# Performance work log

Hardware: AMD Instinct MI355X
Metric: run time of the kernel (lower is better)

## Reference

```python
import jax, jax.numpy as jnp
import numpy as np

HIDDEN = 1024
EMB = HIDDEN // 2          # embedding_dim = hidden_dim // 2
NUM_OPS = 8
BATCH = 16384


def setup_inputs() -> dict:
    key = jax.random.key(0)
    ks = jax.random.split(key, 8)
    x = jax.random.normal(ks[0], (BATCH, HIDDEN), dtype=jnp.float32)
    sampled_ops = jax.random.randint(ks[1], (BATCH,), 0, NUM_OPS, dtype=jnp.int32)
    op_emb = jax.random.normal(ks[2], (NUM_OPS, EMB), dtype=jnp.float32) * 0.02
    # per-expert 2-layer MLP params (Linear stored as [in, out] for x @ W)
    s1 = 1.0 / np.sqrt(HIDDEN + EMB)
    s2 = 1.0 / np.sqrt(HIDDEN)
    W1 = jax.random.uniform(ks[3], (NUM_OPS, HIDDEN + EMB, HIDDEN), jnp.float32, -s1, s1)
    b1 = jax.random.uniform(ks[4], (NUM_OPS, HIDDEN), jnp.float32, -s1, s1)
    W2 = jax.random.uniform(ks[5], (NUM_OPS, HIDDEN, HIDDEN), jnp.float32, -s2, s2)
    b2 = jax.random.uniform(ks[6], (NUM_OPS, HIDDEN), jnp.float32, -s2, s2)
    return {"x": x, "sampled_ops": sampled_ops, "op_emb": op_emb,
            "W1": W1, "b1": b1, "W2": W2, "b2": b2}


def reference(x, sampled_ops, op_emb, W1, b1, W2, b2):
    # gather per-token operator embedding and augment input
    emb = jnp.take(op_emb, sampled_ops, axis=0)            # [B, EMB]
    x_aug = jnp.concatenate([x, emb], axis=-1)             # [B, H+EMB]
    num_ops = W1.shape[0]
    out = jnp.zeros_like(x)
    # loop over the small fixed expert set; mask-combine per token
    for o in range(num_ops):
        h = jax.nn.relu(x_aug @ W1[o] + b1[o])             # [B, H]
        y = jax.nn.relu(h @ W2[o] + b2[o])                 # [B, H]
        mask = (sampled_ops == o)[:, None]
        out = out + jnp.where(mask, y, 0.0)
    return out
```

## Files before the change

### kernel.cpp

```cpp
#include <hip/hip_runtime.h>
#include <hip/hip_bf16.h>

#define BATCH 16384
#define HID   1024
#define EMBD  512
#define NOPS  8
#define MAXT  136
#define CNTS  16

typedef __attribute__((ext_vector_type(8))) short bf16x8;
typedef __attribute__((ext_vector_type(4))) float f32x4;

__device__ __forceinline__ unsigned short f2bf(float f) {
  unsigned int u = __float_as_uint(f);
  u += 0x7FFF + ((u >> 16) & 1);
  return (unsigned short)(u >> 16);
}

__device__ __forceinline__ unsigned int pk2(float a, float b) {
  __hip_bfloat162 t = __float22bfloat162_rn(make_float2(a, b));
  return *(unsigned int*)(&t);
}

__device__ __forceinline__ void lds_load16(void* lds, const void* g) {
  __builtin_amdgcn_global_load_lds(
      (const __attribute__((address_space(1))) unsigned int*)g,
      (__attribute__((address_space(3))) unsigned int*)lds, 16, 0, 0);
}

__device__ __forceinline__ void decode_bid(int bid, int& g, int& nx) {
  g = 17 * (bid & 7) + (bid >> 6);
  nx = (bid >> 3) & 7;
}

__device__ __forceinline__ void w_prep_tile(const float* __restrict__ W,
                                            short* __restrict__ Wp,
                                            int ks, int nx, int tid) {
  int n = tid & 127, kh = tid >> 7;
  const float* src = W + (size_t)(ks * 32 + kh * 16) * 1024 + nx * 128 + n;
  float v[16];
#pragma unroll
  for (int kk = 0; kk < 16; ++kk) v[kk] = src[(size_t)kk * 1024];
  uint4 a, b;
  a.x = pk2(v[0], v[1]);  a.y = pk2(v[2], v[3]);
  a.z = pk2(v[4], v[5]);  a.w = pk2(v[6], v[7]);
  b.x = pk2(v[8], v[9]);  b.y = pk2(v[10], v[11]);
  b.z = pk2(v[12], v[13]); b.w = pk2(v[14], v[15]);
  uint4* dst = (uint4*)Wp;
  dst[(2 * kh) * 128 + n]     = a;
  dst[(2 * kh + 1) * 128 + n] = b;
}

__global__ void bucket_ce_k(const int* __restrict__ ops, int* __restrict__ cnt,
                            int* __restrict__ idx, const float* __restrict__ W1,
                            const float* __restrict__ emb,
                            const float* __restrict__ b1, float* __restrict__ ce,
                            short* __restrict__ W1p, const float* __restrict__ x,
                            unsigned int* __restrict__ xb) {
  int bid = blockIdx.x;
  int tid = threadIdx.x;
  if (bid >= 2240) {
    size_t i = ((size_t)(bid - 2240) * 256 + tid) * 16;
    const float4* src = (const float4*)(x + i);
    float4 f0 = src[0], f1 = src[1], f2v = src[2], f3 = src[3];
    uint4 p0 = make_uint4(pk2(f0.x, f0.y), pk2(f0.z, f0.w),
                          pk2(f1.x, f1.y), pk2(f1.z, f1.w));
    uint4 p1 = make_uint4(pk2(f2v.x, f2v.y), pk2(f2v.z, f2v.w),
                          pk2(f3.x, f3.y), pk2(f3.z, f3.w));
    uint4* dst = (uint4*)(xb + i / 2);
    dst[0] = p0;
    dst[1] = p1;
    return;
  }
  if (bid >= 192) {
    int b = bid - 192;
    int e = b / 256; int rr = b % 256; int nx = rr / 32, ks = rr % 32;
    w_prep_tile(W1 + (size_t)e * 1536 * 1024,
                W1p + ((size_t)(e * 8 + nx) * 32 + ks) * 4096, ks, nx, tid);
    return;
  }
  if (bid >= 64) {
    int cb = bid - 64;
    int e = cb >> 4, kp = cb & 15;
    int n = tid * 4;
    const float* Wc = W1 + (size_t)e * 1536 * 1024 + (size_t)(1024 + kp * 32) * 1024 + n;
    const float* ee = emb + e * EMBD + kp * 32;
    float4 a = make_float4(0.f, 0.f, 0.f, 0.f);
#pragma unroll
    for (int kk = 0; kk < 32; ++kk) {
      float s = ee[kk];
      float4 r = *(const float4*)(Wc + (size_t)kk * 1024);
      a.x += s * r.x; a.y += s * r.y; a.z += s * r.z; a.w += s * r.w;
    }
    if (kp == 0) {
      float4 b = *(const float4*)(b1 + e * HID + n);
      a.x += b.x; a.y += b.y; a.z += b.z; a.w += b.w;
    }
    float* d = ce + e * HID + n;
    atomicAdd(d + 0, a.x); atomicAdd(d + 1, a.y);
    atomicAdd(d + 2, a.z); atomicAdd(d + 3, a.w);
    return;
  }
  __shared__ int wcnt[4][NOPS];
  __shared__ int wbase[4][NOPS];
  int lane = tid & 63, w = tid >> 6;
  int t = bid * 256 + tid;
  int op = ops[t];
  unsigned long long msave = 0;
#pragma unroll
  for (int o = 0; o < NOPS; ++o) {
    unsigned long long mm = __ballot(op == o);
    if (op == o) msave = mm;
    if (lane == o) wcnt[w][o] = __popcll(mm);
  }
  __syncthreads();
  if (tid < NOPS) {
    int c0 = wcnt[0][tid], c1 = wcnt[1][tid], c2 = wcnt[2][tid], c3 = wcnt[3][tid];
    int base = atomicAdd(&cnt[tid * CNTS], c0 + c1 + c2 + c3);
    wbase[0][tid] = base;
    wbase[1][tid] = base + c0;
    wbase[2][tid] = base + c0 + c1;
    wbase[3][tid] = base + c0 + c1 + c2;
  }
  __syncthreads();
  int pre = __popcll(msave & ((1ull << lane) - 1ull));
  idx[op * BATCH + wbase[w][op] + pre] = t;
}

__global__ void schedule_k(const int* __restrict__ cnt, int* __restrict__ desc,
                           int* __restrict__ ntp, int* __restrict__ idx) {
  __shared__ int base[NOPS + 1];
  int tid = threadIdx.x;
  if (tid == 0) {
    int n = 0;
    for (int e = 0; e < NOPS; ++e) { base[e] = n; n += (cnt[e * CNTS] + 127) >> 7; }
    base[NOPS] = n;
    *ntp = n;
  }
  __syncthreads();
  for (int e = 0; e < NOPS; ++e) {
    int b0 = base[e], nt = base[e + 1] - b0;
    for (int t = tid; t < nt; t += 256) {
      desc[2 * (b0 + t)] = e;
      desc[2 * (b0 + t) + 1] = t * 128;
    }
  }
  for (int e = 0; e < NOPS; ++e) {
    int c = cnt[e * CNTS];
    int cp = (c + 127) & ~127;
    for (int p = c + tid; p < cp; p += 256) idx[e * BATCH + p] = 0;
  }
}

__global__ __launch_bounds__(256) void gemm1_w2_k(
    const unsigned int* __restrict__ xb, const int* __restrict__ idx,
    const float* __restrict__ ce, const short* __restrict__ W1p,
    unsigned short* __restrict__ hp, const int* __restrict__ desc,
    const int* __restrict__ ntp, const float* __restrict__ W2,
    short* __restrict__ W2p) {
  int bid = blockIdx.x;
  int tid = threadIdx.x;
  if (bid >= 8 * MAXT) {
    int b = bid - 8 * MAXT;
    int e = b / 256; int rr = b % 256; int nx = rr / 32, ks = rr % 32;
    w_prep_tile(W2 + (size_t)e * 1024 * 1024,
                W2p + ((size_t)(e * 8 + nx) * 32 + ks) * 4096, ks, nx, tid);
    return;
  }
  int g, nx;
  decode_bid(bid, g, nx);
  if (g >= *ntp) return;
  int e = desc[2 * g], rs = desc[2 * g + 1];

  __shared__ __align__(16) char smem[16384];
  short* lA = (short*)smem;
  short* lB = (short*)(smem + 8192);

  int lane = tid & 63, w = tid >> 6;
  int wm = w >> 1, wn = w & 1;
  int fr = lane & 15, fq = lane >> 4;

  int t0 = idx[e * BATCH + rs + lane];
  int t1 = idx[e * BATCH + rs + 64 + lane];
  const char* a0 = (const char*)xb + (size_t)t0 * 2048 + w * 16;
  const char* a1 = (const char*)xb + (size_t)t1 * 2048 + w * 16;
  const char* Bsrc = (const char*)W1p + (size_t)(e * 8 + nx) * 32 * 8192;

  f32x4 acc[4][4] = {};

  for (int ks = 0; ks < 32; ++ks) {
    const char* bs = Bsrc + ks * 8192;
    lds_load16(smem + w * 2048,        a0 + ks * 64);
    lds_load16(smem + w * 2048 + 1024, a1 + ks * 64);
    lds_load16(smem + 8192 + w * 1024, bs + w * 1024 + lane * 16);
    lds_load16(smem + 12288 + w * 1024, bs + 4096 + w * 1024 + lane * 16);
    __syncthreads();

    bf16x8 af[4], bfr[4];
#pragma unroll
    for (int i = 0; i < 4; ++i)
      af[i] = *(const bf16x8*)&lA[(fq * 128 + wm * 64 + i * 16 + fr) * 8];
#pragma unroll
    for (int j = 0; j < 4; ++j)
      bfr[j] = *(const bf16x8*)&lB[(fq * 128 + wn * 64 + j * 16 + fr) * 8];
#pragma unroll
    for (int i = 0; i < 4; ++i)
#pragma unroll
      for (int j = 0; j < 4; ++j)
        acc[i][j] = __builtin_amdgcn_mfma_f32_16x16x32_bf16(af[i], bfr[j], acc[i][j], 0, 0, 0);
    __syncthreads();
  }

  float bias[4];
#pragma unroll
  for (int j = 0; j < 4; ++j)
    bias[j] = ce[e * HID + nx * 128 + wn * 64 + j * 16 + fr];

  int lr = lane >> 2;
#pragma unroll
  for (int i = 0; i < 4; ++i) {
    __syncthreads();
#pragma unroll
    for (int j = 0; j < 4; ++j)
#pragma unroll
      for (int rg = 0; rg < 4; ++rg) {
        float v = acc[i][j][rg] + bias[j];
        v = v > 0.f ? v : 0.f;
        int row16 = fq * 4 + rg;
        int off = w * 2048 + row16 * 128 + (j * 16 + fr) * 2;
        off ^= (row16 & 1) << 6;
        *(unsigned short*)(smem + off) = f2bf(v);
      }
    __syncthreads();
    int R = wm * 64 + i * 16 + lr;
#pragma unroll
    for (int s = 0; s < 2; ++s) {
      int ch = (lane & 3) + s * 4;
      int off = w * 2048 + lr * 128 + ch * 16;
      off ^= (lr & 1) << 6;
      uint4 val = *(const uint4*)(smem + off);
      int ks2 = nx * 4 + wn * 2 + (ch >> 2);
      int kq = ch & 3;
      *(uint4*)(hp + (((size_t)(g * 32 + ks2) * 4 + kq) * 128 + R) * 8) = val;
    }
  }
}

__global__ __launch_bounds__(256) void gemm2_k(
    const unsigned short* __restrict__ hp, const float* __restrict__ b2,
    const short* __restrict__ W2p, float* __restrict__ out,
    const int* __restrict__ idx, const int* __restrict__ cnt,
    const int* __restrict__ desc, const int* __restrict__ ntp) {
  int g, nx;
  decode_bid(blockIdx.x, g, nx);
  if (g >= *ntp) return;
  int e = desc[2 * g], rs = desc[2 * g + 1];
  int ce2 = cnt[e * CNTS];

  __shared__ __align__(16) char smem[16384];
  __shared__ int toks[128];
  short* lA = (short*)smem;
  short* lB = (short*)(smem + 8192);

  int tid = threadIdx.x, lane = tid & 63, w = tid >> 6;
  int wm = w >> 1, wn = w & 1;
  int fr = lane & 15, fq = lane >> 4;

  if (tid < 128) toks[tid] = idx[e * BATCH + rs + tid];

  const char* Asrc = (const char*)hp + (size_t)g * 32 * 8192;
  const char* Bsrc = (const char*)W2p + (size_t)(e * 8 + nx) * 32 * 8192;

  f32x4 acc[4][4] = {};

  for (int ks = 0; ks < 32; ++ks) {
    const char* as = Asrc + ks * 8192;
    const char* bs = Bsrc + ks * 8192;
    lds_load16(smem + w * 1024, as + w * 1024 + lane * 16);
    lds_load16(smem + 4096 + w * 1024, as + 4096 + w * 1024 + lane * 16);
    lds_load16(smem + 8192 + w * 1024, bs + w * 1024 + lane * 16);
    lds_load16(smem + 12288 + w * 1024, bs + 4096 + w * 1024 + lane * 16);
    __syncthreads();

    bf16x8 af[4], bfr[4];
#pragma unroll
    for (int i = 0; i < 4; ++i)
      af[i] = *(const bf16x8*)&lA[(fq * 128 + wm * 64 + i * 16 + fr) * 8];
#pragma unroll
    for (int j = 0; j < 4; ++j)
      bfr[j] = *(const bf16x8*)&lB[(fq * 128 + wn * 64 + j * 16 + fr) * 8];
#pragma unroll
    for (int i = 0; i < 4; ++i)
#pragma unroll
      for (int j = 0; j < 4; ++j)
        acc[i][j] = __builtin_amdgcn_mfma_f32_16x16x32_bf16(af[i], bfr[j], acc[i][j], 0, 0, 0);
    __syncthreads();
  }

  float bias[4];
#pragma unroll
  for (int j = 0; j < 4; ++j)
    bias[j] = b2[e * HID + nx * 128 + wn * 64 + j * 16 + fr];

  int lr = lane >> 2;
#pragma unroll
  for (int i = 0; i < 4; ++i) {
    __syncthreads();
#pragma unroll
    for (int j = 0; j < 4; ++j)
#pragma unroll
      for (int rg = 0; rg < 4; ++rg) {
        float v = acc[i][j][rg] + bias[j];
        int row16 = fq * 4 + rg;
        int off = w * 4096 + row16 * 256 + (j * 16 + fr) * 4;
        off ^= (row16 & 1) << 6;
        *(float*)(smem + off) = v > 0.f ? v : 0.f;
      }
    __syncthreads();
    int R = wm * 64 + i * 16 + lr;
    if (R < ce2 - rs) {
      float* orow = out + (size_t)toks[R] * HID + nx * 128 + wn * 64;
#pragma unroll
      for (int s = 0; s < 4; ++s) {
        int ch = (lane & 3) + s * 4;
        int off = w * 4096 + lr * 256 + ch * 16;
        off ^= (lr & 1) << 6;
        *(float4*)(orow + ch * 4) = *(const float4*)(smem + off);
      }
    }
  }
}


extern "C" void kernel_launch(void* const* d_in, const int* in_sizes, int n_in,
                              void* d_out, int out_size, void* d_ws, size_t ws_size,
                              hipStream_t stream) {
  const float* x   = (const float*)d_in[0];
  const int*   ops = (const int*)d_in[1];
  const float* emb = (const float*)d_in[2];
  const float* W1  = (const float*)d_in[3];
  const float* b1  = (const float*)d_in[4];
  const float* W2  = (const float*)d_in[5];
  const float* b2  = (const float*)d_in[6];
  float* out = (float*)d_out;

  char* ws = (char*)d_ws;
  int* cnt  = (int*)(ws + 0);
  float* ce = (float*)(ws + 512);
  int* ntp  = (int*)(ws + 33280);
  int* desc = (int*)(ws + 33344);
  int* idx  = (int*)(ws + 36864);
  short* W1p = (short*)(ws + 561152);
  short* W2p = (short*)(ws + 17338368);
  unsigned short* hp = (unsigned short*)(ws + 34115584);
  unsigned int* xb = (unsigned int*)(ws + 69767168);

  hipMemsetAsync(ws, 0, 33280, stream);
  bucket_ce_k<<<2240 + 4096, 256, 0, stream>>>(ops, cnt, idx, W1, emb, b1, ce, W1p, x, xb);
  schedule_k<<<1, 256, 0, stream>>>(cnt, desc, ntp, idx);
  gemm1_w2_k<<<8 * MAXT + 2048, 256, 0, stream>>>(xb, idx, ce, W1p, hp, desc, ntp, W2, W2p);
  gemm2_k<<<8 * MAXT, 256, 0, stream>>>(hp, b2, W2p, out, idx, cnt, desc, ntp);
}
```

Baseline: 301.7 us.

## Double-buffer LDS tiles in both expert GEMM kernels to overlap loads with MFMA

After: 307.1 us. No clear change (+1.8%).

```diff
diff --git a/kernel.cpp b/kernel.cpp
--- a/kernel.cpp
+++ b/kernel.cpp
@@ -172,9 +172,7 @@
   if (g >= *ntp) return;
   int e = desc[2 * g], rs = desc[2 * g + 1];
 
-  __shared__ __align__(16) char smem[16384];
-  short* lA = (short*)smem;
-  short* lB = (short*)(smem + 8192);
+  __shared__ __align__(16) char smem[32768];
 
   int lane = tid & 63, w = tid >> 6;
   int wm = w >> 1, wn = w & 1;
@@ -186,16 +184,27 @@
   const char* a1 = (const char*)xb + (size_t)t1 * 2048 + w * 16;
   const char* Bsrc = (const char*)W1p + (size_t)(e * 8 + nx) * 32 * 8192;
 
+  lds_load16(smem + w * 2048,         a0);
+  lds_load16(smem + w * 2048 + 1024,  a1);
+  lds_load16(smem + 8192 + w * 1024,  Bsrc + w * 1024 + lane * 16);
+  lds_load16(smem + 12288 + w * 1024, Bsrc + 4096 + w * 1024 + lane * 16);
+  asm volatile("s_waitcnt vmcnt(0)" ::: "memory");
+  __builtin_amdgcn_s_barrier();
+
   f32x4 acc[4][4] = {};
 
   for (int ks = 0; ks < 32; ++ks) {
-    const char* bs = Bsrc + ks * 8192;
-    lds_load16(smem + w * 2048,        a0 + ks * 64);
-    lds_load16(smem + w * 2048 + 1024, a1 + ks * 64);
-    lds_load16(smem + 8192 + w * 1024, bs + w * 1024 + lane * 16);
-    lds_load16(smem + 12288 + w * 1024, bs + 4096 + w * 1024 + lane * 16);
-    __syncthreads();
-
+    int cur = ks & 1;
+    char* nb = smem + (cur ^ 1) * 16384;
+    if (ks < 31) {
+      const char* bs = Bsrc + (ks + 1) * 8192;
+      lds_load16(nb + w * 2048,         a0 + (ks + 1) * 64);
+      lds_load16(nb + w * 2048 + 1024,  a1 + (ks + 1) * 64);
+      lds_load16(nb + 8192 + w * 1024,  bs + w * 1024 + lane * 16);
+      lds_load16(nb + 12288 + w * 1024, bs + 4096 + w * 1024 + lane * 16);
+    }
+    const short* lA = (const short*)(smem + cur * 16384);
+    const short* lB = (const short*)(smem + cur * 16384 + 8192);
     bf16x8 af[4], bfr[4];
 #pragma unroll
     for (int i = 0; i < 4; ++i)
@@ -208,7 +217,8 @@
 #pragma unroll
       for (int j = 0; j < 4; ++j)
         acc[i][j] = __builtin_amdgcn_mfma_f32_16x16x32_bf16(af[i], bfr[j], acc[i][j], 0, 0, 0);
-    __syncthreads();
+    asm volatile("s_waitcnt vmcnt(0)" ::: "memory");
+    __builtin_amdgcn_s_barrier();
   }
 
   float bias[4];
@@ -257,10 +267,8 @@
   int e = desc[2 * g], rs = desc[2 * g + 1];
   int ce2 = cnt[e * CNTS];
 
-  __shared__ __align__(16) char smem[16384];
+  __shared__ __align__(16) char smem[32768];
   __shared__ int toks[128];
-  short* lA = (short*)smem;
-  short* lB = (short*)(smem + 8192);
 
   int tid = threadIdx.x, lane = tid & 63, w = tid >> 6;
   int wm = w >> 1, wn = w & 1;
@@ -271,17 +279,28 @@
   const char* Asrc = (const char*)hp + (size_t)g * 32 * 8192;
   const char* Bsrc = (const char*)W2p + (size_t)(e * 8 + nx) * 32 * 8192;
 
+  lds_load16(smem + w * 1024,         Asrc + w * 1024 + lane * 16);
+  lds_load16(smem + 4096 + w * 1024,  Asrc + 4096 + w * 1024 + lane * 16);
+  lds_load16(smem + 8192 + w * 1024,  Bsrc + w * 1024 + lane * 16);
+  lds_load16(smem + 12288 + w * 1024, Bsrc + 4096 + w * 1024 + lane * 16);
+  asm volatile("s_waitcnt vmcnt(0)" ::: "memory");
+  __builtin_amdgcn_s_barrier();
+
   f32x4 acc[4][4] = {};
 
   for (int ks = 0; ks < 32; ++ks) {
-    const char* as = Asrc + ks * 8192;
-    const char* bs = Bsrc + ks * 8192;
-    lds_load16(smem + w * 1024, as + w * 1024 + lane * 16);
-    lds_load16(smem + 4096 + w * 1024, as + 4096 + w * 1024 + lane * 16);
-    lds_load16(smem + 8192 + w * 1024, bs + w * 1024 + lane * 16);
-    lds_load16(smem + 12288 + w * 1024, bs + 4096 + w * 1024 + lane * 16);
-    __syncthreads();
-
+    int cur = ks & 1;
+    char* nb = smem + (cur ^ 1) * 16384;
+    if (ks < 31) {
+      const char* as = Asrc + (ks + 1) * 8192;
+      const char* bs = Bsrc + (ks + 1) * 8192;
+      lds_load16(nb + w * 1024,         as + w * 1024 + lane * 16);
+      lds_load16(nb + 4096 + w * 1024,  as + 4096 + w * 1024 + lane * 16);
+      lds_load16(nb + 8192 + w * 1024,  bs + w * 1024 + lane * 16);
+      lds_load16(nb + 12288 + w * 1024, bs + 4096 + w * 1024 + lane * 16);
+    }
+    const short* lA = (const short*)(smem + cur * 16384);
+    const short* lB = (const short*)(smem + cur * 16384 + 8192);
     bf16x8 af[4], bfr[4];
 #pragma unroll
     for (int i = 0; i < 4; ++i)
@@ -294,7 +313,8 @@
 #pragma unroll
       for (int j = 0; j < 4; ++j)
         acc[i][j] = __builtin_amdgcn_mfma_f32_16x16x32_bf16(af[i], bfr[j], acc[i][j], 0, 0, 0);
-    __syncthreads();
+    asm volatile("s_waitcnt vmcnt(0)" ::: "memory");
+    __builtin_amdgcn_s_barrier();
   }
 
   float bias[4];
```

## Double-buffer LDS in both GEMMs and fold tile scheduling into kernels

Applied to the files above, without the earlier changes.

Result: no change. 304.2 us (+0.8%).

```diff
diff --git a/kernel.cpp b/kernel.cpp
--- a/kernel.cpp
+++ b/kernel.cpp
@@ -31,6 +31,20 @@
 __device__ __forceinline__ void decode_bid(int bid, int& g, int& nx) {
   g = 17 * (bid & 7) + (bid >> 6);
   nx = (bid >> 3) & 7;
+}
+
+__device__ __forceinline__ int decode_tile(const int* __restrict__ cnt,
+                                           int g, int& rs, int& ce_cnt) {
+  int e = -1, at = 0;
+  rs = 0; ce_cnt = 0;
+#pragma unroll
+  for (int o = 0; o < NOPS; ++o) {
+    int c = cnt[o * CNTS];
+    int t = (c + 127) >> 7;
+    if (e < 0 && g < at + t) { e = o; rs = (g - at) * 128; ce_cnt = c; }
+    at += t;
+  }
+  return e;
 }
 
 __device__ __forceinline__ void w_prep_tile(const float* __restrict__ W,
@@ -127,37 +141,11 @@
   idx[op * BATCH + wbase[w][op] + pre] = t;
 }
 
-__global__ void schedule_k(const int* __restrict__ cnt, int* __restrict__ desc,
-                           int* __restrict__ ntp, int* __restrict__ idx) {
-  __shared__ int base[NOPS + 1];
-  int tid = threadIdx.x;
-  if (tid == 0) {
-    int n = 0;
-    for (int e = 0; e < NOPS; ++e) { base[e] = n; n += (cnt[e * CNTS] + 127) >> 7; }
-    base[NOPS] = n;
-    *ntp = n;
-  }
-  __syncthreads();
-  for (int e = 0; e < NOPS; ++e) {
-    int b0 = base[e], nt = base[e + 1] - b0;
-    for (int t = tid; t < nt; t += 256) {
-      desc[2 * (b0 + t)] = e;
-      desc[2 * (b0 + t) + 1] = t * 128;
-    }
-  }
-  for (int e = 0; e < NOPS; ++e) {
-    int c = cnt[e * CNTS];
-    int cp = (c + 127) & ~127;
-    for (int p = c + tid; p < cp; p += 256) idx[e * BATCH + p] = 0;
-  }
-}
-
 __global__ __launch_bounds__(256) void gemm1_w2_k(
     const unsigned int* __restrict__ xb, const int* __restrict__ idx,
     const float* __restrict__ ce, const short* __restrict__ W1p,
-    unsigned short* __restrict__ hp, const int* __restrict__ desc,
-    const int* __restrict__ ntp, const float* __restrict__ W2,
-    short* __restrict__ W2p) {
+    unsigned short* __restrict__ hp, const int* __restrict__ cnt,
+    const float* __restrict__ W2, short* __restrict__ W2p) {
   int bid = blockIdx.x;
   int tid = threadIdx.x;
   if (bid >= 8 * MAXT) {
@@ -169,47 +157,67 @@
   }
   int g, nx;
   decode_bid(bid, g, nx);
-  if (g >= *ntp) return;
-  int e = desc[2 * g], rs = desc[2 * g + 1];
-
-  __shared__ __align__(16) char smem[16384];
-  short* lA = (short*)smem;
-  short* lB = (short*)(smem + 8192);
+  int rs, ce_cnt;
+  int e = decode_tile(cnt, g, rs, ce_cnt);
+  if (e < 0) return;
+
+  __shared__ __align__(16) char smem[32768];
+  char* s0 = smem;
+  char* s1 = smem + 16384;
 
   int lane = tid & 63, w = tid >> 6;
   int wm = w >> 1, wn = w & 1;
   int fr = lane & 15, fq = lane >> 4;
 
-  int t0 = idx[e * BATCH + rs + lane];
-  int t1 = idx[e * BATCH + rs + 64 + lane];
+  int p0 = rs + lane, p1 = rs + 64 + lane;
+  int t0 = (p0 < ce_cnt) ? idx[e * BATCH + p0] : 0;
+  int t1 = (p1 < ce_cnt) ? idx[e * BATCH + p1] : 0;
   const char* a0 = (const char*)xb + (size_t)t0 * 2048 + w * 16;
   const char* a1 = (const char*)xb + (size_t)t1 * 2048 + w * 16;
   const char* Bsrc = (const char*)W1p + (size_t)(e * 8 + nx) * 32 * 8192;
 
+  lds_load16(s0 + w * 2048,         a0);
+  lds_load16(s0 + w * 2048 + 1024,  a1);
+  lds_load16(s0 + 8192 + w * 1024,  Bsrc + w * 1024 + lane * 16);
+  lds_load16(s0 + 12288 + w * 1024, Bsrc + 4096 + w * 1024 + lane * 16);
+  asm volatile("s_waitcnt vmcnt(0)" ::: "memory");
+  __builtin_amdgcn_s_barrier();
+
   f32x4 acc[4][4] = {};
-
-  for (int ks = 0; ks < 32; ++ks) {
-    const char* bs = Bsrc + ks * 8192;
-    lds_load16(smem + w * 2048,        a0 + ks * 64);
-    lds_load16(smem + w * 2048 + 1024, a1 + ks * 64);
-    lds_load16(smem + 8192 + w * 1024, bs + w * 1024 + lane * 16);
-    lds_load16(smem + 12288 + w * 1024, bs + 4096 + w * 1024 + lane * 16);
-    __syncthreads();
-
-    bf16x8 af[4], bfr[4];
-#pragma unroll
-    for (int i = 0; i < 4; ++i)
-      af[i] = *(const bf16x8*)&lA[(fq * 128 + wm * 64 + i * 16 + fr) * 8];
-#pragma unroll
-    for (int j = 0; j < 4; ++j)
-      bfr[j] = *(const bf16x8*)&lB[(fq * 128 + wn * 64 + j * 16 + fr) * 8];
-#pragma unroll
-    for (int i = 0; i < 4; ++i)
-#pragma unroll
-      for (int j = 0; j < 4; ++j)
-        acc[i][j] = __builtin_amdgcn_mfma_f32_16x16x32_bf16(af[i], bfr[j], acc[i][j], 0, 0, 0);
-    __syncthreads();
-  }
+  int fo = (fq * 128 + wm * 64 + fr) * 8;
+  int bo = (fq * 128 + wn * 64 + fr) * 8;
+
+#define G1_STEP(CURB, NXTB, KS)                                               \
+  {                                                                           \
+    if ((KS) < 31) {                                                          \
+      const char* bs_ = Bsrc + ((KS) + 1) * 8192;                             \
+      lds_load16((NXTB) + w * 2048,         a0 + ((KS) + 1) * 64);            \
+      lds_load16((NXTB) + w * 2048 + 1024,  a1 + ((KS) + 1) * 64);            \
+      lds_load16((NXTB) + 8192 + w * 1024,  bs_ + w * 1024 + lane * 16);      \
+      lds_load16((NXTB) + 12288 + w * 1024, bs_ + 4096 + w * 1024 + lane * 16); \
+    }                                                                         \
+    const short* lA_ = (const short*)(CURB);                                  \
+    const short* lB_ = (const short*)((CURB) + 8192);                         \
+    bf16x8 af[4], bfr[4];                                                     \
+    _Pragma("unroll")                                                         \
+    for (int i = 0; i < 4; ++i) af[i] = *(const bf16x8*)&lA_[fo + i * 128];   \
+    _Pragma("unroll")                                                         \
+    for (int j = 0; j < 4; ++j) bfr[j] = *(const bf16x8*)&lB_[bo + j * 128];  \
+    _Pragma("unroll")                                                         \
+    for (int i = 0; i < 4; ++i)                                               \
+      _Pragma("unroll")                                                       \
+      for (int j = 0; j < 4; ++j)                                             \
+        acc[i][j] = __builtin_amdgcn_mfma_f32_16x16x32_bf16(af[i], bfr[j],    \
+                                                            acc[i][j], 0, 0, 0); \
+    asm volatile("s_waitcnt vmcnt(0)" ::: "memory");                          \
+    __builtin_amdgcn_s_barrier();                                             \
+  }
+
+  for (int ks = 0; ks < 32; ks += 2) {
+    G1_STEP(s0, s1, ks);
+    G1_STEP(s1, s0, ks + 1);
+  }
+#undef G1_STEP
 
   float bias[4];
 #pragma unroll
@@ -249,53 +257,73 @@
 __global__ __launch_bounds__(256) void gemm2_k(
     const unsigned short* __restrict__ hp, const float* __restrict__ b2,
     const short* __restrict__ W2p, float* __restrict__ out,
-    const int* __restrict__ idx, const int* __restrict__ cnt,
-    const int* __restrict__ desc, const int* __restrict__ ntp) {
+    const int* __restrict__ idx, const int* __restrict__ cnt) {
   int g, nx;
   decode_bid(blockIdx.x, g, nx);
-  if (g >= *ntp) return;
-  int e = desc[2 * g], rs = desc[2 * g + 1];
-  int ce2 = cnt[e * CNTS];
-
-  __shared__ __align__(16) char smem[16384];
+  int rs, ce_cnt;
+  int e = decode_tile(cnt, g, rs, ce_cnt);
+  if (e < 0) return;
+
+  __shared__ __align__(16) char smem[32768];
   __shared__ int toks[128];
-  short* lA = (short*)smem;
-  short* lB = (short*)(smem + 8192);
+  char* s0 = smem;
+  char* s1 = smem + 16384;
 
   int tid = threadIdx.x, lane = tid & 63, w = tid >> 6;
   int wm = w >> 1, wn = w & 1;
   int fr = lane & 15, fq = lane >> 4;
 
-  if (tid < 128) toks[tid] = idx[e * BATCH + rs + tid];
+  if (tid < 128) {
+    int p = rs + tid;
+    toks[tid] = (p < ce_cnt) ? idx[e * BATCH + p] : 0;
+  }
 
   const char* Asrc = (const char*)hp + (size_t)g * 32 * 8192;
   const char* Bsrc = (const char*)W2p + (size_t)(e * 8 + nx) * 32 * 8192;
 
+  lds_load16(s0 + w * 1024,         Asrc + w * 1024 + lane * 16);
+  lds_load16(s0 + 4096 + w * 1024,  Asrc + 4096 + w * 1024 + lane * 16);
+  lds_load16(s0 + 8192 + w * 1024,  Bsrc + w * 1024 + lane * 16);
+  lds_load16(s0 + 12288 + w * 1024, Bsrc + 4096 + w * 1024 + lane * 16);
+  asm volatile("s_waitcnt vmcnt(0)" ::: "memory");
+  __builtin_amdgcn_s_barrier();
+
   f32x4 acc[4][4] = {};
-
-  for (int ks = 0; ks < 32; ++ks) {
-    const char* as = Asrc + ks * 8192;
-    const char* bs = Bsrc + ks * 8192;
-    lds_load16(smem + w * 1024, as + w * 1024 + lane * 16);
-    lds_load16(smem + 4096 + w * 1024, as + 4096 + w * 1024 + lane * 16);
-    lds_load16(smem + 8192 + w * 1024, bs + w * 1024 + lane * 16);
-    lds_load16(smem + 12288 + w * 1024, bs + 4096 + w * 1024 + lane * 16);
-    __syncthreads();
-
-    bf16x8 af[4], bfr[4];
-#pragma unroll
-    for (int i = 0; i < 4; ++i)
-      af[i] = *(const bf16x8*)&lA[(fq * 128 + wm * 64 + i * 16 + fr) * 8];
-#pragma unroll
-    for (int j = 0; j < 4; ++j)
-      bfr[j] = *(const bf16x8*)&lB[(fq * 128 + wn * 64 + j * 16 + fr) * 8];
-#pragma unroll
-    for (int i = 0; i < 4; ++i)
-#pragma unroll
-      for (int j = 0; j < 4; ++j)
-        acc[i][j] = __builtin_amdgcn_mfma_f32_16x16x32_bf16(af[i], bfr[j], acc[i][j], 0, 0, 0);
-    __syncthreads();
-  }
+  int fo = (fq * 128 + wm * 64 + fr) * 8;
+  int bo = (fq * 128 + wn * 64 + fr) * 8;
+
+#define G2_STEP(CURB, NXTB, KS)                                               \
+  {                                                                           \
+    if ((KS) < 31) {                                                          \
+      const char* as_ = Asrc + ((KS) + 1) * 8192;                             \
+      const char* bs_ = Bsrc + ((KS) + 1) * 8192;                             \
+      lds_load16((NXTB) + w * 1024,         as_ + w * 1024 + lane * 16);      \
+      lds_load16((NXTB) + 4096 + w * 1024,  as_ + 4096 + w * 1024 + lane * 16); \
+      lds_load16((NXTB) + 8192 + w * 1024,  bs_ + w * 1024 + lane * 16);      \
+      lds_load16((NXTB) + 12288 + w * 1024, bs_ + 4096 + w * 1024 + lane * 16); \
+    }                                                                         \
+    const short* lA_ = (const short*)(CURB);                                  \
+    const short* lB_ = (const short*)((CURB) + 8192);                         \
+    bf16x8 af[4], bfr[4];                                                     \
+    _Pragma("unroll")                                                         \
+    for (int i = 0; i < 4; ++i) af[i] = *(const bf16x8*)&lA_[fo + i * 128];   \
+    _Pragma("unroll")                                                         \
+    for (int j = 0; j < 4; ++j) bfr[j] = *(const bf16x8*)&lB_[bo + j * 128];  \
+    _Pragma("unroll")                                                         \
+    for (int i = 0; i < 4; ++i)                                               \
+      _Pragma("unroll")                                                       \
+      for (int j = 0; j < 4; ++j)                                             \
+        acc[i][j] = __builtin_amdgcn_mfma_f32_16x16x32_bf16(af[i], bfr[j],    \
+                                                            acc[i][j], 0, 0, 0); \
+    asm volatile("s_waitcnt vmcnt(0)" ::: "memory");                          \
+    __builtin_amdgcn_s_barrier();                                             \
+  }
+
+  for (int ks = 0; ks < 32; ks += 2) {
+    G2_STEP(s0, s1, ks);
+    G2_STEP(s1, s0, ks + 1);
+  }
+#undef G2_STEP
 
   float bias[4];
 #pragma unroll
@@ -318,7 +346,7 @@
       }
     __syncthreads();
     int R = wm * 64 + i * 16 + lr;
-    if (R < ce2 - rs) {
+    if (R < ce_cnt - rs) {
       float* orow = out + (size_t)toks[R] * HID + nx * 128 + wn * 64;
 #pragma unroll
       for (int s = 0; s < 4; ++s) {
@@ -347,8 +375,6 @@
   char* ws = (char*)d_ws;
   int* cnt  = (int*)(ws + 0);
   float* ce = (float*)(ws + 512);
-  int* ntp  = (int*)(ws + 33280);
-  int* desc = (int*)(ws + 33344);
   int* idx  = (int*)(ws + 36864);
   short* W1p = (short*)(ws + 561152);
   short* W2p = (short*)(ws + 17338368);
@@ -357,7 +383,6 @@
 
   hipMemsetAsync(ws, 0, 33280, stream);
   bucket_ce_k<<<2240 + 4096, 256, 0, stream>>>(ops, cnt, idx, W1, emb, b1, ce, W1p, x, xb);
-  schedule_k<<<1, 256, 0, stream>>>(cnt, desc, ntp, idx);
-  gemm1_w2_k<<<8 * MAXT + 2048, 256, 0, stream>>>(xb, idx, ce, W1p, hp, desc, ntp, W2, W2p);
-  gemm2_k<<<8 * MAXT, 256, 0, stream>>>(hp, b2, W2p, out, idx, cnt, desc, ntp);
-}
+  gemm1_w2_k<<<8 * MAXT + 2048, 256, 0, stream>>>(xb, idx, ce, W1p, hp, cnt, W2, W2p);
+  gemm2_k<<<8 * MAXT, 256, 0, stream>>>(hp, b2, W2p, out, idx, cnt);
+}
```
